# Kernel optimization log

Measured on AMD Instinct MI355X. Metric: run time of the kernel, lower is better.

The kernel has to match this reference:

```python
import jax, jax.numpy as jnp
import numpy as np

# Block-diagonal SplitMLP: fc1 group g sees [day | items[g]]; fc2 is purely per-group.
B, C, V, H, O, G = 128, 16, 32, 64, 4, 10000


def setup_inputs() -> dict:
    key = jax.random.key(0)
    ks = jax.random.split(key, 7)
    bound1 = 1.0 / np.sqrt(C + V * G)   # nn.Linear init bound for fc1 (full fan-in)
    bound2 = 1.0 / np.sqrt(H * G)       # fc2 fan-in
    return {
        "day": jax.random.normal(ks[0], (B, C), jnp.float32),
        "items": jax.random.normal(ks[1], (B, G, V), jnp.float32),
        "W1_day": jax.random.uniform(ks[2], (G, H, C), jnp.float32, -bound1, bound1),
        "W1_var": jax.random.uniform(ks[3], (G, H, V), jnp.float32, -bound1, bound1),
        "b1": jax.random.uniform(ks[4], (G, H), jnp.float32, -bound1, bound1),
        "W2": jax.random.uniform(ks[5], (G, O, H), jnp.float32, -bound2, bound2),
        "b2": jax.random.uniform(ks[6], (G, O), jnp.float32, -bound2, bound2),
    }


def reference(day, items, W1_day, W1_var, b1, W2, b2):
    # fc1: shared day columns + per-group var block, then ReLU
    h = (
        jnp.einsum("bc,ghc->bgh", day, W1_day)
        + jnp.einsum("bgv,ghv->bgh", items, W1_var)
        + b1
    )
    h = jax.nn.relu(h)
    # fc2: purely block-diagonal (num_const = 0)
    y = jnp.einsum("bgh,goh->bgo", h, W2) + b2  # (B, G, O)
    return y
```

## Files before the change

kernel.cpp:

```cpp
#include <hip/hip_runtime.h>
#include <hip/hip_bf16.h>


typedef __bf16 v8bf __attribute__((ext_vector_type(8)));
typedef float  v4f  __attribute__((ext_vector_type(4)));

#define B_  128
#define C_  16
#define V_  32
#define H_  64
#define O_  4
#define G_  10000
#define HS  104

__device__ __forceinline__ v8bf cvt8(float4 lo, float4 hi) {
  v8bf r;
  r[0] = (__bf16)lo.x; r[1] = (__bf16)lo.y; r[2] = (__bf16)lo.z; r[3] = (__bf16)lo.w;
  r[4] = (__bf16)hi.x; r[5] = (__bf16)hi.y; r[6] = (__bf16)hi.z; r[7] = (__bf16)hi.w;
  return r;
}

__device__ __forceinline__ v8bf gload8(const float* __restrict__ p) {
  const float4* p4 = reinterpret_cast<const float4*>(p);
  float4 lo = p4[0];
  float4 hi = p4[1];
  return cvt8(lo, hi);
}

__global__ __launch_bounds__(256, 6)
void splitmlp_kernel(const float* __restrict__ day,
                     const float* __restrict__ items,
                     const float* __restrict__ W1d,
                     const float* __restrict__ W1v,
                     const float* __restrict__ b1,
                     const float* __restrict__ W2,
                     const float* __restrict__ b2,
                     float* __restrict__ out) {
  __shared__ __bf16 Hbuf[B_ * HS];

  const int t    = threadIdx.x;
  const int g    = blockIdx.x;
  const int w    = t >> 6;
  const int lane = t & 63;
  const int c    = lane & 15;
  const int q    = lane >> 4;
  const int r0   = w * 32;
  const int bA0  = r0 + c;
  const int bA1  = bA0 + 16;

  const size_t gV   = (size_t)g * V_;
  const float* W1dg = W1d + (size_t)g * (H_ * C_);
  const float* W1vg = W1v + (size_t)g * (H_ * V_);

  v8bf zf;
#pragma unroll
  for (int i = 0; i < 8; ++i) zf[i] = (__bf16)0.0f;
  v4f zero = {0.f, 0.f, 0.f, 0.f};

  float bias[4];
#pragma unroll
  for (int n = 0; n < 4; ++n) bias[n] = b1[(size_t)g * H_ + n * 16 + c];

  v4f acc[2][4];
#pragma unroll
  for (int m = 0; m < 2; ++m)
#pragma unroll
    for (int n = 0; n < 4; ++n) acc[m][n] = zero;

#pragma unroll
  for (int kt = 0; kt < 2; ++kt) {
    const int  k0    = kt * 32 + q * 8;
    const bool isday = (k0 < 16);
    const bool valid = (k0 < 48);

    const float* pa0 = isday ? (day + bA0 * C_ + k0)
                     : valid ? (items + (size_t)bA0 * (G_ * V_) + gV + (k0 - 16))
                             : day;
    const float* pa1 = isday ? (day + bA1 * C_ + k0)
                     : valid ? (items + (size_t)bA1 * (G_ * V_) + gV + (k0 - 16))
                             : day;
    v8bf a0 = gload8(pa0);
    v8bf a1 = gload8(pa1);
    if (!valid) { a0 = zf; a1 = zf; }

#pragma unroll
    for (int n = 0; n < 4; ++n) {
      const int h = n * 16 + c;
      const float* pw = isday ? (W1dg + h * C_ + k0)
                      : valid ? (W1vg + h * V_ + (k0 - 16))
                              : day;
      v8bf bw = gload8(pw);
      acc[0][n] = __builtin_amdgcn_mfma_f32_16x16x32_bf16(a0, bw, acc[0][n], 0, 0, 0);
      acc[1][n] = __builtin_amdgcn_mfma_f32_16x16x32_bf16(a1, bw, acc[1][n], 0, 0, 0);
    }
  }

#pragma unroll
  for (int n = 0; n < 4; ++n)
#pragma unroll
    for (int m = 0; m < 2; ++m)
#pragma unroll
      for (int r = 0; r < 4; ++r) {
        float v = fmaxf(acc[m][n][r] + bias[n], 0.0f);
        Hbuf[(r0 + m * 16 + q * 4 + r) * HS + n * 16 + c] = (__bf16)v;
      }

  v4f y0 = zero, y1 = zero;
#pragma unroll
  for (int kt = 0; kt < 2; ++kt) {
    const int k0 = kt * 32 + q * 8;
    const float* pw2 = (c < O_) ? (W2 + (size_t)g * (O_ * H_) + c * H_ + k0) : day;
    v8bf wf = gload8(pw2);
    if (c >= O_) wf = zf;
    v8bf h0 = *reinterpret_cast<const v8bf*>(&Hbuf[(r0 + c) * HS + k0]);
    v8bf h1 = *reinterpret_cast<const v8bf*>(&Hbuf[(r0 + 16 + c) * HS + k0]);
    y0 = __builtin_amdgcn_mfma_f32_16x16x32_bf16(wf, h0, y0, 0, 0, 0);
    y1 = __builtin_amdgcn_mfma_f32_16x16x32_bf16(wf, h1, y1, 0, 0, 0);
  }

  if (q == 0) {
    const float4 b2v = *reinterpret_cast<const float4*>(b2 + (size_t)g * O_);
    float4 o0, o1;
    o0.x = y0[0] + b2v.x; o0.y = y0[1] + b2v.y; o0.z = y0[2] + b2v.z; o0.w = y0[3] + b2v.w;
    o1.x = y1[0] + b2v.x; o1.y = y1[1] + b2v.y; o1.z = y1[2] + b2v.z; o1.w = y1[3] + b2v.w;
    *reinterpret_cast<float4*>(out + (size_t)(r0 + c) * (G_ * O_) + (size_t)g * O_) = o0;
    *reinterpret_cast<float4*>(out + (size_t)(r0 + 16 + c) * (G_ * O_) + (size_t)g * O_) = o1;
  }
}

extern "C" void kernel_launch(void* const* d_in, const int* in_sizes, int n_in,
                              void* d_out, int out_size, void* d_ws, size_t ws_size,
                              hipStream_t stream) {
  const float* day   = (const float*)d_in[0];
  const float* items = (const float*)d_in[1];
  const float* W1d   = (const float*)d_in[2];
  const float* W1v   = (const float*)d_in[3];
  const float* b1    = (const float*)d_in[4];
  const float* W2    = (const float*)d_in[5];
  const float* b2    = (const float*)d_in[6];
  float* out = (float*)d_out;
  splitmlp_kernel<<<G_, 256, 0, stream>>>(day, items, W1d, W1v, b1, W2, b2, out);
}
```

Baseline: 395.2 us.

## Process eight groups per block and batch output stores across four groups

Each thread block now handles eight consecutive groups in an unrolled loop instead of one group per block, cutting the grid to G/8 blocks. For each group, all global loads (activations, fc1 weights and fc2 weights) are issued before the bf16 conversion and MFMA work, so loads are exposed up front. Outputs for four consecutive groups are kept in registers and written as 64 contiguous bytes per row, instead of scattered 16-byte stores. The cost is heavier register use (launch bounds lowered to 4 blocks per CU), a large unrolled body, and fewer blocks to spread across CUs.

```diff
diff --git a/kernel.cpp b/kernel.cpp
--- a/kernel.cpp
+++ b/kernel.cpp
@@ -5,13 +5,14 @@
 typedef __bf16 v8bf __attribute__((ext_vector_type(8)));
 typedef float  v4f  __attribute__((ext_vector_type(4)));
 
-#define B_  128
-#define C_  16
-#define V_  32
-#define H_  64
-#define O_  4
-#define G_  10000
-#define HS  104
+#define B_   128
+#define C_   16
+#define V_   32
+#define H_   64
+#define O_   4
+#define G_   10000
+#define GPB  8
+#define HS   104
 
 __device__ __forceinline__ v8bf cvt8(float4 lo, float4 hi) {
   v8bf r;
@@ -20,14 +21,7 @@
   return r;
 }
 
-__device__ __forceinline__ v8bf gload8(const float* __restrict__ p) {
-  const float4* p4 = reinterpret_cast<const float4*>(p);
-  float4 lo = p4[0];
-  float4 hi = p4[1];
-  return cvt8(lo, hi);
-}
-
-__global__ __launch_bounds__(256, 6)
+__global__ __launch_bounds__(256, 4)
 void splitmlp_kernel(const float* __restrict__ day,
                      const float* __restrict__ items,
                      const float* __restrict__ W1d,
@@ -39,7 +33,7 @@
   __shared__ __bf16 Hbuf[B_ * HS];
 
   const int t    = threadIdx.x;
-  const int g    = blockIdx.x;
+  const int g0   = blockIdx.x * GPB;
   const int w    = t >> 6;
   const int lane = t & 63;
   const int c    = lane & 15;
@@ -48,83 +42,114 @@
   const int bA0  = r0 + c;
   const int bA1  = bA0 + 16;
 
-  const size_t gV   = (size_t)g * V_;
-  const float* W1dg = W1d + (size_t)g * (H_ * C_);
-  const float* W1vg = W1v + (size_t)g * (H_ * V_);
-
   v8bf zf;
 #pragma unroll
   for (int i = 0; i < 8; ++i) zf[i] = (__bf16)0.0f;
   v4f zero = {0.f, 0.f, 0.f, 0.f};
 
-  float bias[4];
-#pragma unroll
-  for (int n = 0; n < 4; ++n) bias[n] = b1[(size_t)g * H_ + n * 16 + c];
-
-  v4f acc[2][4];
-#pragma unroll
-  for (int m = 0; m < 2; ++m)
-#pragma unroll
-    for (int n = 0; n < 4; ++n) acc[m][n] = zero;
+  float4 o0[4], o1[4];
 
 #pragma unroll
-  for (int kt = 0; kt < 2; ++kt) {
-    const int  k0    = kt * 32 + q * 8;
-    const bool isday = (k0 < 16);
-    const bool valid = (k0 < 48);
+  for (int gi = 0; gi < GPB; ++gi) {
+    const int g = g0 + gi;
+    const float* W1dg = W1d + (size_t)g * (H_ * C_);
+    const float* W1vg = W1v + (size_t)g * (H_ * V_);
+    const float* W2g  = W2  + (size_t)g * (O_ * H_);
+    const size_t gV   = (size_t)g * V_;
 
-    const float* pa0 = isday ? (day + bA0 * C_ + k0)
-                     : valid ? (items + (size_t)bA0 * (G_ * V_) + gV + (k0 - 16))
-                             : day;
-    const float* pa1 = isday ? (day + bA1 * C_ + k0)
-                     : valid ? (items + (size_t)bA1 * (G_ * V_) + gV + (k0 - 16))
-                             : day;
-    v8bf a0 = gload8(pa0);
-    v8bf a1 = gload8(pa1);
-    if (!valid) { a0 = zf; a1 = zf; }
+    float4 Af[2][2][2];
+    float4 Bf[2][4][2];
+    float4 Wf[2][2];
+#pragma unroll
+    for (int kt = 0; kt < 2; ++kt) {
+      const int  k0    = kt * 32 + q * 8;
+      const bool isday = (k0 < 16);
+      const bool valid = (k0 < 48);
+      const float* pa0 = isday ? (day + bA0 * C_ + k0)
+                       : valid ? (items + (size_t)bA0 * (G_ * V_) + gV + (k0 - 16))
+                               : day;
+      const float* pa1 = isday ? (day + bA1 * C_ + k0)
+                       : valid ? (items + (size_t)bA1 * (G_ * V_) + gV + (k0 - 16))
+                               : day;
+      Af[0][kt][0] = reinterpret_cast<const float4*>(pa0)[0];
+      Af[0][kt][1] = reinterpret_cast<const float4*>(pa0)[1];
+      Af[1][kt][0] = reinterpret_cast<const float4*>(pa1)[0];
+      Af[1][kt][1] = reinterpret_cast<const float4*>(pa1)[1];
+#pragma unroll
+      for (int n = 0; n < 4; ++n) {
+        const int h = n * 16 + c;
+        const float* pw = isday ? (W1dg + h * C_ + k0)
+                        : valid ? (W1vg + h * V_ + (k0 - 16))
+                                : day;
+        Bf[kt][n][0] = reinterpret_cast<const float4*>(pw)[0];
+        Bf[kt][n][1] = reinterpret_cast<const float4*>(pw)[1];
+      }
+      const float* pw2 = (c < O_) ? (W2g + c * H_ + k0) : day;
+      Wf[kt][0] = reinterpret_cast<const float4*>(pw2)[0];
+      Wf[kt][1] = reinterpret_cast<const float4*>(pw2)[1];
+    }
+    float bias[4];
+#pragma unroll
+    for (int n = 0; n < 4; ++n) bias[n] = b1[(size_t)g * H_ + n * 16 + c];
+    const float4 b2v = *reinterpret_cast<const float4*>(b2 + (size_t)g * O_);
 
+    v8bf a[2][2], bw[2][4], wf[2];
 #pragma unroll
-    for (int n = 0; n < 4; ++n) {
-      const int h = n * 16 + c;
-      const float* pw = isday ? (W1dg + h * C_ + k0)
-                      : valid ? (W1vg + h * V_ + (k0 - 16))
-                              : day;
-      v8bf bw = gload8(pw);
-      acc[0][n] = __builtin_amdgcn_mfma_f32_16x16x32_bf16(a0, bw, acc[0][n], 0, 0, 0);
-      acc[1][n] = __builtin_amdgcn_mfma_f32_16x16x32_bf16(a1, bw, acc[1][n], 0, 0, 0);
+    for (int kt = 0; kt < 2; ++kt) {
+      const int  k0    = kt * 32 + q * 8;
+      const bool valid = (k0 < 48);
+      a[0][kt] = valid ? cvt8(Af[0][kt][0], Af[0][kt][1]) : zf;
+      a[1][kt] = valid ? cvt8(Af[1][kt][0], Af[1][kt][1]) : zf;
+#pragma unroll
+      for (int n = 0; n < 4; ++n) bw[kt][n] = cvt8(Bf[kt][n][0], Bf[kt][n][1]);
+      wf[kt] = (c < O_) ? cvt8(Wf[kt][0], Wf[kt][1]) : zf;
     }
-  }
 
-#pragma unroll
-  for (int n = 0; n < 4; ++n)
+    v4f acc[2][4];
 #pragma unroll
     for (int m = 0; m < 2; ++m)
 #pragma unroll
-      for (int r = 0; r < 4; ++r) {
-        float v = fmaxf(acc[m][n][r] + bias[n], 0.0f);
-        Hbuf[(r0 + m * 16 + q * 4 + r) * HS + n * 16 + c] = (__bf16)v;
+      for (int n = 0; n < 4; ++n) acc[m][n] = zero;
+#pragma unroll
+    for (int kt = 0; kt < 2; ++kt)
+#pragma unroll
+      for (int n = 0; n < 4; ++n) {
+        acc[0][n] = __builtin_amdgcn_mfma_f32_16x16x32_bf16(a[0][kt], bw[kt][n], acc[0][n], 0, 0, 0);
+        acc[1][n] = __builtin_amdgcn_mfma_f32_16x16x32_bf16(a[1][kt], bw[kt][n], acc[1][n], 0, 0, 0);
       }
 
-  v4f y0 = zero, y1 = zero;
 #pragma unroll
-  for (int kt = 0; kt < 2; ++kt) {
-    const int k0 = kt * 32 + q * 8;
-    const float* pw2 = (c < O_) ? (W2 + (size_t)g * (O_ * H_) + c * H_ + k0) : day;
-    v8bf wf = gload8(pw2);
-    if (c >= O_) wf = zf;
-    v8bf h0 = *reinterpret_cast<const v8bf*>(&Hbuf[(r0 + c) * HS + k0]);
-    v8bf h1 = *reinterpret_cast<const v8bf*>(&Hbuf[(r0 + 16 + c) * HS + k0]);
-    y0 = __builtin_amdgcn_mfma_f32_16x16x32_bf16(wf, h0, y0, 0, 0, 0);
-    y1 = __builtin_amdgcn_mfma_f32_16x16x32_bf16(wf, h1, y1, 0, 0, 0);
-  }
+    for (int n = 0; n < 4; ++n)
+#pragma unroll
+      for (int m = 0; m < 2; ++m)
+#pragma unroll
+        for (int r = 0; r < 4; ++r) {
+          float v = fmaxf(acc[m][n][r] + bias[n], 0.0f);
+          Hbuf[(r0 + m * 16 + q * 4 + r) * HS + n * 16 + c] = (__bf16)v;
+        }
 
-  if (q == 0) {
-    const float4 b2v = *reinterpret_cast<const float4*>(b2 + (size_t)g * O_);
-    float4 o0, o1;
-    o0.x = y0[0] + b2v.x; o0.y = y0[1] + b2v.y; o0.z = y0[2] + b2v.z; o0.w = y0[3] + b2v.w;
-    o1.x = y1[0] + b2v.x; o1.y = y1[1] + b2v.y; o1.z = y1[2] + b2v.z; o1.w = y1[3] + b2v.w;
-    *reinterpret_cast<float4*>(out + (size_t)(r0 + c) * (G_ * O_) + (size_t)g * O_) = o0;
-    *reinterpret_cast<float4*>(out + (size_t)(r0 + 16 + c) * (G_ * O_) + (size_t)g * O_) = o1;
+    v4f y0 = zero, y1 = zero;
+#pragma unroll
+    for (int kt = 0; kt < 2; ++kt) {
+      const int k0 = kt * 32 + q * 8;
+      v8bf h0 = *reinterpret_cast<const v8bf*>(&Hbuf[(r0 + c) * HS + k0]);
+      v8bf h1 = *reinterpret_cast<const v8bf*>(&Hbuf[(r0 + 16 + c) * HS + k0]);
+      y0 = __builtin_amdgcn_mfma_f32_16x16x32_bf16(wf[kt], h0, y0, 0, 0, 0);
+      y1 = __builtin_amdgcn_mfma_f32_16x16x32_bf16(wf[kt], h1, y1, 0, 0, 0);
+    }
+    const int s = gi & 3;
+    o0[s].x = y0[0] + b2v.x; o0[s].y = y0[1] + b2v.y; o0[s].z = y0[2] + b2v.z; o0[s].w = y0[3] + b2v.w;
+    o1[s].x = y1[0] + b2v.x; o1[s].y = y1[1] + b2v.y; o1[s].z = y1[2] + b2v.z; o1[s].w = y1[3] + b2v.w;
+
+    if (s == 3 && q == 0) {
+      const size_t gbase = (size_t)(g0 + (gi & ~3)) * O_;
+      float* p0 = out + (size_t)(r0 + c) * (G_ * O_) + gbase;
+      float* p1 = out + (size_t)(r0 + 16 + c) * (G_ * O_) + gbase;
+#pragma unroll
+      for (int j = 0; j < 4; ++j) reinterpret_cast<float4*>(p0)[j] = o0[j];
+#pragma unroll
+      for (int j = 0; j < 4; ++j) reinterpret_cast<float4*>(p1)[j] = o1[j];
+    }
   }
 }
 
@@ -139,5 +164,5 @@
   const float* W2    = (const float*)d_in[5];
   const float* b2    = (const float*)d_in[6];
   float* out = (float*)d_out;
-  splitmlp_kernel<<<G_, 256, 0, stream>>>(day, items, W1d, W1v, b1, W2, b2, out);
+  splitmlp_kernel<<<(G_ + GPB - 1) / GPB, 256, 0, stream>>>(day, items, W1d, W1v, b1, W2, b2, out);
 }
```

Measured after the change: 456.2 us. +15.5%, slower.

## Process four groups per block with LDS-staged weights and coalesced output

Applied to the files above, without the earlier changes.

Each block now handles four consecutive groups instead of one. W1 for the next group is prefetched into registers while the current group's W1 is staged as bf16 in LDS. The MFMA operands are swapped so weights form the A side and batch the B side. Outputs for the four groups are gathered in LDS and written as contiguous 64-byte runs per batch row, replacing scattered 16-byte stores. This trades more LDS, extra barriers and lower occupancy (launch bounds 4 instead of 6) for better write coalescing and less per-block overhead.

```diff
diff --git a/kernel.cpp b/kernel.cpp
--- a/kernel.cpp
+++ b/kernel.cpp
@@ -3,31 +3,37 @@
 
 
 typedef __bf16 v8bf __attribute__((ext_vector_type(8)));
+typedef __bf16 v4bf __attribute__((ext_vector_type(4)));
 typedef float  v4f  __attribute__((ext_vector_type(4)));
 
-#define B_  128
-#define C_  16
-#define V_  32
-#define H_  64
-#define O_  4
-#define G_  10000
-#define HS  104
+#define B_   128
+#define C_   16
+#define V_   32
+#define H_   64
+#define O_   4
+#define G_   10000
+#define GPB  4
+#define WS_  56
+#define HS_  72
+#define YS_  20
 
+__device__ __forceinline__ v4bf cvt4(float4 f) {
+  v4bf r;
+  r[0] = (__bf16)f.x; r[1] = (__bf16)f.y; r[2] = (__bf16)f.z; r[3] = (__bf16)f.w;
+  return r;
+}
 __device__ __forceinline__ v8bf cvt8(float4 lo, float4 hi) {
   v8bf r;
   r[0] = (__bf16)lo.x; r[1] = (__bf16)lo.y; r[2] = (__bf16)lo.z; r[3] = (__bf16)lo.w;
   r[4] = (__bf16)hi.x; r[5] = (__bf16)hi.y; r[6] = (__bf16)hi.z; r[7] = (__bf16)hi.w;
   return r;
 }
-
 __device__ __forceinline__ v8bf gload8(const float* __restrict__ p) {
   const float4* p4 = reinterpret_cast<const float4*>(p);
-  float4 lo = p4[0];
-  float4 hi = p4[1];
-  return cvt8(lo, hi);
+  return cvt8(p4[0], p4[1]);
 }
 
-__global__ __launch_bounds__(256, 6)
+__global__ __launch_bounds__(256, 4)
 void splitmlp_kernel(const float* __restrict__ day,
                      const float* __restrict__ items,
                      const float* __restrict__ W1d,
@@ -36,95 +42,133 @@
                      const float* __restrict__ W2,
                      const float* __restrict__ b2,
                      float* __restrict__ out) {
-  __shared__ __bf16 Hbuf[B_ * HS];
+  __shared__ __bf16 W1s[H_ * WS_];
+  __shared__ __bf16 Hb[4][32 * HS_];
+  __shared__ float  Yb[B_ * YS_];
 
   const int t    = threadIdx.x;
-  const int g    = blockIdx.x;
+  const int g0   = blockIdx.x * GPB;
   const int w    = t >> 6;
   const int lane = t & 63;
   const int c    = lane & 15;
   const int q    = lane >> 4;
-  const int r0   = w * 32;
-  const int bA0  = r0 + c;
-  const int bA1  = bA0 + 16;
-
-  const size_t gV   = (size_t)g * V_;
-  const float* W1dg = W1d + (size_t)g * (H_ * C_);
-  const float* W1vg = W1v + (size_t)g * (H_ * V_);
+  const int wbase = w * 32;
 
   v8bf zf;
 #pragma unroll
   for (int i = 0; i < 8; ++i) zf[i] = (__bf16)0.0f;
-  v4f zero = {0.f, 0.f, 0.f, 0.f};
+  const v4f zero = {0.f, 0.f, 0.f, 0.f};
 
-  float bias[4];
+  float4 pd, pv0, pv1;
+  {
+    const float* W1dg = W1d + (size_t)g0 * (H_ * C_);
+    const float* W1vg = W1v + (size_t)g0 * (H_ * V_);
+    pd  = reinterpret_cast<const float4*>(W1dg)[t];
+    pv0 = reinterpret_cast<const float4*>(W1vg)[t];
+    pv1 = reinterpret_cast<const float4*>(W1vg)[t + 256];
+  }
+
+#pragma unroll 1
+  for (int gi = 0; gi < GPB; ++gi) {
+    const int g = g0 + gi;
+
+    __syncthreads();
+    {
+      const int hd = t >> 2, kd = (t & 3) << 2;
+      *reinterpret_cast<v4bf*>(&W1s[hd * WS_ + kd]) = cvt4(pd);
+      const int hv0 = t >> 3, kv0 = C_ + ((t & 7) << 2);
+      *reinterpret_cast<v4bf*>(&W1s[hv0 * WS_ + kv0]) = cvt4(pv0);
+      const int i2 = t + 256;
+      const int hv1 = i2 >> 3, kv1 = C_ + ((i2 & 7) << 2);
+      *reinterpret_cast<v4bf*>(&W1s[hv1 * WS_ + kv1]) = cvt4(pv1);
+    }
+    if (gi < GPB - 1) {
+      const float* W1dn = W1d + (size_t)(g + 1) * (H_ * C_);
+      const float* W1vn = W1v + (size_t)(g + 1) * (H_ * V_);
+      pd  = reinterpret_cast<const float4*>(W1dn)[t];
+      pv0 = reinterpret_cast<const float4*>(W1vn)[t];
+      pv1 = reinterpret_cast<const float4*>(W1vn)[t + 256];
+    }
+    __syncthreads();
+
+    v8bf bfrag[2][2];
 #pragma unroll
-  for (int n = 0; n < 4; ++n) bias[n] = b1[(size_t)g * H_ + n * 16 + c];
+    for (int nb = 0; nb < 2; ++nb) {
+      const int b = wbase + nb * 16 + c;
+      const float* pit = items + (size_t)b * (G_ * V_) + (size_t)g * V_;
+      const float* p0 = (q < 2) ? (day + b * C_ + q * 8) : (pit + (q - 2) * 8);
+      bfrag[nb][0] = gload8(p0);
+      bfrag[nb][1] = (q < 2) ? gload8(pit + 16 + q * 8) : zf;
+    }
 
-  v4f acc[2][4];
+    v8bf wfrag[4][2];
 #pragma unroll
-  for (int m = 0; m < 2; ++m)
+    for (int m = 0; m < 4; ++m) {
+      const int row = (m * 16 + c) * WS_;
+      wfrag[m][0] = *reinterpret_cast<const v8bf*>(&W1s[row + q * 8]);
+      wfrag[m][1] = (q < 2) ? *reinterpret_cast<const v8bf*>(&W1s[row + 32 + q * 8]) : zf;
+    }
+
+    v4f acc[4][2];
 #pragma unroll
-    for (int n = 0; n < 4; ++n) acc[m][n] = zero;
+    for (int m = 0; m < 4; ++m)
+#pragma unroll
+      for (int nb = 0; nb < 2; ++nb) acc[m][nb] = zero;
+#pragma unroll
+    for (int m = 0; m < 4; ++m)
+#pragma unroll
+      for (int nb = 0; nb < 2; ++nb) {
+        acc[m][nb] = __builtin_amdgcn_mfma_f32_16x16x32_bf16(wfrag[m][0], bfrag[nb][0], acc[m][nb], 0, 0, 0);
+        acc[m][nb] = __builtin_amdgcn_mfma_f32_16x16x32_bf16(wfrag[m][1], bfrag[nb][1], acc[m][nb], 0, 0, 0);
+      }
 
 #pragma unroll
-  for (int kt = 0; kt < 2; ++kt) {
-    const int  k0    = kt * 32 + q * 8;
-    const bool isday = (k0 < 16);
-    const bool valid = (k0 < 48);
+    for (int m = 0; m < 4; ++m) {
+      const float4 bb = *reinterpret_cast<const float4*>(b1 + (size_t)g * H_ + m * 16 + q * 4);
+#pragma unroll
+      for (int nb = 0; nb < 2; ++nb) {
+        v4bf hv;
+        hv[0] = (__bf16)fmaxf(acc[m][nb][0] + bb.x, 0.f);
+        hv[1] = (__bf16)fmaxf(acc[m][nb][1] + bb.y, 0.f);
+        hv[2] = (__bf16)fmaxf(acc[m][nb][2] + bb.z, 0.f);
+        hv[3] = (__bf16)fmaxf(acc[m][nb][3] + bb.w, 0.f);
+        *reinterpret_cast<v4bf*>(&Hb[w][(nb * 16 + c) * HS_ + m * 16 + q * 4]) = hv;
+      }
+    }
 
-    const float* pa0 = isday ? (day + bA0 * C_ + k0)
-                     : valid ? (items + (size_t)bA0 * (G_ * V_) + gV + (k0 - 16))
-                             : day;
-    const float* pa1 = isday ? (day + bA1 * C_ + k0)
-                     : valid ? (items + (size_t)bA1 * (G_ * V_) + gV + (k0 - 16))
-                             : day;
-    v8bf a0 = gload8(pa0);
-    v8bf a1 = gload8(pa1);
-    if (!valid) { a0 = zf; a1 = zf; }
+    v4f y[2] = {zero, zero};
+#pragma unroll
+    for (int kt = 0; kt < 2; ++kt) {
+      const float* pw2 = W2 + (size_t)g * (O_ * H_) + c * H_ + kt * 32 + q * 8;
+      v8bf w2f = (c < O_) ? gload8(pw2) : zf;
+#pragma unroll
+      for (int nb = 0; nb < 2; ++nb) {
+        v8bf hf = *reinterpret_cast<const v8bf*>(&Hb[w][(nb * 16 + c) * HS_ + kt * 32 + q * 8]);
+        y[nb] = __builtin_amdgcn_mfma_f32_16x16x32_bf16(w2f, hf, y[nb], 0, 0, 0);
+      }
+    }
 
+    if (q == 0) {
+      const float4 b2v = *reinterpret_cast<const float4*>(b2 + (size_t)g * O_);
 #pragma unroll
-    for (int n = 0; n < 4; ++n) {
-      const int h = n * 16 + c;
-      const float* pw = isday ? (W1dg + h * C_ + k0)
-                      : valid ? (W1vg + h * V_ + (k0 - 16))
-                              : day;
-      v8bf bw = gload8(pw);
-      acc[0][n] = __builtin_amdgcn_mfma_f32_16x16x32_bf16(a0, bw, acc[0][n], 0, 0, 0);
-      acc[1][n] = __builtin_amdgcn_mfma_f32_16x16x32_bf16(a1, bw, acc[1][n], 0, 0, 0);
+      for (int nb = 0; nb < 2; ++nb) {
+        const int b = wbase + nb * 16 + c;
+        float4 o;
+        o.x = y[nb][0] + b2v.x;
+        o.y = y[nb][1] + b2v.y;
+        o.z = y[nb][2] + b2v.z;
+        o.w = y[nb][3] + b2v.w;
+        *reinterpret_cast<float4*>(&Yb[b * YS_ + gi * 4]) = o;
+      }
     }
   }
 
+  __syncthreads();
 #pragma unroll
-  for (int n = 0; n < 4; ++n)
-#pragma unroll
-    for (int m = 0; m < 2; ++m)
-#pragma unroll
-      for (int r = 0; r < 4; ++r) {
-        float v = fmaxf(acc[m][n][r] + bias[n], 0.0f);
-        Hbuf[(r0 + m * 16 + q * 4 + r) * HS + n * 16 + c] = (__bf16)v;
-      }
-
-  v4f y0 = zero, y1 = zero;
-#pragma unroll
-  for (int kt = 0; kt < 2; ++kt) {
-    const int k0 = kt * 32 + q * 8;
-    const float* pw2 = (c < O_) ? (W2 + (size_t)g * (O_ * H_) + c * H_ + k0) : day;
-    v8bf wf = gload8(pw2);
-    if (c >= O_) wf = zf;
-    v8bf h0 = *reinterpret_cast<const v8bf*>(&Hbuf[(r0 + c) * HS + k0]);
-    v8bf h1 = *reinterpret_cast<const v8bf*>(&Hbuf[(r0 + 16 + c) * HS + k0]);
-    y0 = __builtin_amdgcn_mfma_f32_16x16x32_bf16(wf, h0, y0, 0, 0, 0);
-    y1 = __builtin_amdgcn_mfma_f32_16x16x32_bf16(wf, h1, y1, 0, 0, 0);
-  }
-
-  if (q == 0) {
-    const float4 b2v = *reinterpret_cast<const float4*>(b2 + (size_t)g * O_);
-    float4 o0, o1;
-    o0.x = y0[0] + b2v.x; o0.y = y0[1] + b2v.y; o0.z = y0[2] + b2v.z; o0.w = y0[3] + b2v.w;
-    o1.x = y1[0] + b2v.x; o1.y = y1[1] + b2v.y; o1.z = y1[2] + b2v.z; o1.w = y1[3] + b2v.w;
-    *reinterpret_cast<float4*>(out + (size_t)(r0 + c) * (G_ * O_) + (size_t)g * O_) = o0;
-    *reinterpret_cast<float4*>(out + (size_t)(r0 + 16 + c) * (G_ * O_) + (size_t)g * O_) = o1;
+  for (int i = t; i < 512; i += 256) {
+    const int b = i >> 2, c4 = i & 3;
+    const float4 v = *reinterpret_cast<const float4*>(&Yb[b * YS_ + c4 * 4]);
+    *reinterpret_cast<float4*>(out + (size_t)b * (G_ * O_) + (size_t)g0 * O_ + c4 * 4) = v;
   }
 }
 
@@ -139,5 +183,5 @@
   const float* W2    = (const float*)d_in[5];
   const float* b2    = (const float*)d_in[6];
   float* out = (float*)d_out;
-  splitmlp_kernel<<<G_, 256, 0, stream>>>(day, items, W1d, W1v, b1, W2, b2, out);
+  splitmlp_kernel<<<G_ / GPB, 256, 0, stream>>>(day, items, W1d, W1v, b1, W2, b2, out);
 }
```

Measured after the change: 352.8 us. 1.12x faster.
